# Kernel tuning notes

Measured on AMD Instinct MI355X. Metric: run time of the kernel, lower is better.

Reference implementation:

```python
import jax, jax.numpy as jnp
import numpy as np

B, P, TL = 2, 256, 1280          # batch, prefix len, text len
H, HEADS, HD = 1024, 16, 64      # hidden, heads, head_dim
NL, V = 2, 32000                 # layers, vocab


def layernorm(x, g, b, eps=1e-5):
    mu = jnp.mean(x, axis=-1, keepdims=True)
    var = jnp.mean((x - mu) ** 2, axis=-1, keepdims=True)
    return (x - mu) / jnp.sqrt(var + eps) * g + b


def setup_inputs() -> dict:
    key = jax.random.key(0)
    ks = jax.random.split(key, 12)
    s = 0.02
    return {
        "prefix_embeds": jax.random.normal(ks[0], (B, P, H), jnp.float32),
        "text_ids": jax.random.randint(ks[1], (B, TL), 0, V),
        "embed": jax.random.normal(ks[2], (V, H), jnp.float32) * s,
        "Wq": jax.random.normal(ks[3], (NL, H, H), jnp.float32) * s,
        "Wk": jax.random.normal(ks[4], (NL, H, H), jnp.float32) * s,
        "Wv": jax.random.normal(ks[5], (NL, H, H), jnp.float32) * s,
        "Wo": jax.random.normal(ks[6], (NL, H, H), jnp.float32) * s,
        "g1": jnp.ones((NL, H), jnp.float32),
        "b1": jnp.zeros((NL, H), jnp.float32),
        "g2": jnp.ones((NL, H), jnp.float32),
        "b2": jnp.zeros((NL, H), jnp.float32),
        "W1": jax.random.normal(ks[7], (NL, H, 4 * H), jnp.float32) * s,
        "bm1": jnp.zeros((NL, 4 * H), jnp.float32),
        "W2": jax.random.normal(ks[8], (NL, 4 * H, H), jnp.float32) * s,
        "bm2": jnp.zeros((NL, H), jnp.float32),
        "gf": jnp.ones((H,), jnp.float32),
        "bf": jnp.zeros((H,), jnp.float32),
        "Whead": jax.random.normal(ks[9], (H, V), jnp.float32) * s,
    }


def reference(prefix_embeds, text_ids, embed, Wq, Wk, Wv, Wo,
              g1, b1, g2, b2, W1, bm1, W2, bm2, gf, bf, Whead):
    x = jnp.concatenate([prefix_embeds, embed[text_ids]], axis=1)  # [B,T,H]
    T = x.shape[1]
    causal = jnp.tril(jnp.ones((T, T), dtype=bool))                # True = keep
    scale = 1.0 / jnp.sqrt(jnp.float32(HD))
    for l in range(NL):
        h = layernorm(x, g1[l], b1[l])
        q = (h @ Wq[l]).reshape(B, T, HEADS, HD).transpose(0, 2, 1, 3)
        k = (h @ Wk[l]).reshape(B, T, HEADS, HD).transpose(0, 2, 1, 3)
        v = (h @ Wv[l]).reshape(B, T, HEADS, HD).transpose(0, 2, 1, 3)
        scores = jnp.einsum('bhqd,bhkd->bhqk', q, k) * scale       # [B,h,T,T]
        scores = jnp.where(causal, scores, -jnp.inf)
        attn = jax.nn.softmax(scores, axis=-1)
        out = jnp.einsum('bhqk,bhkd->bhqd', attn, v)
        out = out.transpose(0, 2, 1, 3).reshape(B, T, H) @ Wo[l]
        x = x + out
        h2 = layernorm(x, g2[l], b2[l])
        x = x + jax.nn.silu(h2 @ W1[l] + bm1[l]) @ W2[l] + bm2[l]
    x = layernorm(x, gf, bf)
    return x @ Whead                                               # [B,T,V]
```

## Files before the change

kernel.cpp:

```cpp
#include <hip/hip_runtime.h>
#include <stdint.h>

#define B_ 2
#define P_ 256
#define TL_ 1280
#define T_ 1536
#define H_ 1024
#define HEADS_ 16
#define HD_ 64
#define NL_ 2
#define V_ 32000
#define F_ 4096
#define BT_ (B_ * T_)

typedef __attribute__((ext_vector_type(4))) float f32x4;
typedef __attribute__((ext_vector_type(8))) short short8;
typedef __attribute__((ext_vector_type(4))) short short4v;

typedef __attribute__((address_space(3))) uint32_t lds_u32_t;
typedef const __attribute__((address_space(1))) uint32_t glb_u32_t;

__device__ inline void gload_lds16(const void* g, void* l) {
    __builtin_amdgcn_global_load_lds((glb_u32_t*)g, (lds_u32_t*)l, 16, 0, 0);
}

__device__ inline short f2bf(float f) {
    union { float f; unsigned u; } v; v.f = f;
    unsigned r = v.u + 0x7FFF + ((v.u >> 16) & 1);
    return (short)(r >> 16);
}

#define BAR() asm volatile("s_barrier" ::: "memory")
#define WAIT_VM0() asm volatile("s_waitcnt vmcnt(0)" ::: "memory")
#define WAIT_VM4() asm volatile("s_waitcnt vmcnt(4)" ::: "memory")
#define WAIT_VM8() asm volatile("s_waitcnt vmcnt(8)" ::: "memory")
#define WAIT_VM32() asm volatile("s_waitcnt vmcnt(32)" ::: "memory")

__global__ __launch_bounds__(256) void k_cvt_all(
    const float* __restrict__ Wq, const float* __restrict__ Wk,
    const float* __restrict__ Wv, const float* __restrict__ Wo,
    const float* __restrict__ W1, const float* __restrict__ W2,
    const float* __restrict__ Wh,
    short* __restrict__ WqkvT, short* __restrict__ WoT,
    short* __restrict__ W1T, short* __restrict__ W2T, short* __restrict__ WhT) {
    int id = blockIdx.x;
    const float* src;
    short* dst;
    int K, N;
    float scale = 1.f;
    if (id < 6144) {
        int mat = id >> 10;
        int tile = id & 1023;
        int l = mat / 3, which = mat - l * 3;
        src = (which == 0 ? Wq : which == 1 ? Wk : Wv) + (size_t)l * H_ * H_;
        dst = WqkvT + (size_t)(l * 3 + which) * H_ * H_;
        K = H_; N = H_;
        if (which == 0) scale = 0.125f;
        id = tile;
    } else if (id < 8192) {
        int rel = id - 6144;
        int l = rel >> 10;
        src = Wo + (size_t)l * H_ * H_;
        dst = WoT + (size_t)l * H_ * H_;
        K = H_; N = H_;
        id = rel & 1023;
    } else if (id < 16384) {
        int rel = id - 8192;
        int l = rel >> 12;
        src = W1 + (size_t)l * H_ * F_;
        dst = W1T + (size_t)l * H_ * F_;
        K = H_; N = F_;
        id = rel & 4095;
    } else if (id < 24576) {
        int rel = id - 16384;
        int l = rel >> 12;
        src = W2 + (size_t)l * F_ * H_;
        dst = W2T + (size_t)l * F_ * H_;
        K = F_; N = H_;
        id = rel & 4095;
    } else {
        id -= 24576;
        src = Wh; dst = WhT;
        K = H_; N = V_;
    }
    int ntn = N >> 5;
    int nb = (id % ntn) * 32, kb = (id / ntn) * 32;

    __shared__ float ts[32][36];
    int tid = threadIdx.x;
    int r = tid >> 3, c4 = (tid & 7) * 4;
    f32x4 v = __builtin_nontemporal_load((const f32x4*)&src[(size_t)(kb + r) * N + nb + c4]);
    *(f32x4*)&ts[r][c4] = v;
    __syncthreads();
    int wn = tid >> 3, wk4 = (tid & 7) * 4;
    short o[4];
#pragma unroll
    for (int j = 0; j < 4; ++j) o[j] = f2bf(ts[wk4 + j][wn] * scale);
    *(short4v*)&dst[(size_t)(nb + wn) * K + kb + wk4] = *(short4v*)o;
}

__global__ __launch_bounds__(256) void k_embed_ln(const float* __restrict__ prefix,
                                                  const int* __restrict__ ids,
                                                  const float* __restrict__ emb,
                                                  const float* __restrict__ g,
                                                  const float* __restrict__ b,
                                                  float* __restrict__ x,
                                                  short* __restrict__ h) {
    int r = blockIdx.x;
    int bb = r / T_, t = r % T_;
    const float* src = (t < P_) ? (prefix + (size_t)(bb * P_ + t) * H_)
                                : (emb + (size_t)ids[bb * TL_ + (t - P_)] * H_);
    int tid = threadIdx.x;
    f32x4 v = *(const f32x4*)&src[tid * 4];
    *(f32x4*)&x[(size_t)r * H_ + tid * 4] = v;
    float s = v[0] + v[1] + v[2] + v[3];
    float sq = v[0] * v[0] + v[1] * v[1] + v[2] * v[2] + v[3] * v[3];
#pragma unroll
    for (int off = 32; off; off >>= 1) {
        s += __shfl_down(s, off, 64);
        sq += __shfl_down(sq, off, 64);
    }
    __shared__ float red[10];
    int wid = tid >> 6;
    if ((tid & 63) == 0) { red[wid] = s; red[4 + wid] = sq; }
    __syncthreads();
    if (tid == 0) {
        float S = red[0] + red[1] + red[2] + red[3];
        float SQ = red[4] + red[5] + red[6] + red[7];
        float mu = S * (1.0f / H_);
        float var = SQ * (1.0f / H_) - mu * mu;
        red[8] = mu;
        red[9] = rsqrtf(var + 1e-5f);
    }
    __syncthreads();
    float mu = red[8], rstd = red[9];
    short o[4];
#pragma unroll
    for (int j = 0; j < 4; ++j)
        o[j] = f2bf((v[j] - mu) * rstd * g[tid * 4 + j] + b[tid * 4 + j]);
    *(short4v*)&h[(size_t)r * H_ + tid * 4] = *(short4v*)o;
}

__global__ __launch_bounds__(256) void k_add_ln(float* __restrict__ x,
                                                const float* __restrict__ p,
                                                const float* __restrict__ g,
                                                const float* __restrict__ b,
                                                short* __restrict__ out) {
    int r = blockIdx.x;
    int tid = threadIdx.x;
    size_t base = (size_t)r * H_ + tid * 4;
    f32x4 v = *(f32x4*)&x[base];
#pragma unroll
    for (int sl = 0; sl < 4; ++sl) {
        f32x4 a = *(const f32x4*)&p[(size_t)sl * BT_ * H_ + base];
#pragma unroll
        for (int j = 0; j < 4; ++j) v[j] += a[j];
    }
    *(f32x4*)&x[base] = v;
    float s = v[0] + v[1] + v[2] + v[3];
    float sq = v[0] * v[0] + v[1] * v[1] + v[2] * v[2] + v[3] * v[3];
#pragma unroll
    for (int off = 32; off; off >>= 1) {
        s += __shfl_down(s, off, 64);
        sq += __shfl_down(sq, off, 64);
    }
    __shared__ float red[10];
    int wid = tid >> 6;
    if ((tid & 63) == 0) { red[wid] = s; red[4 + wid] = sq; }
    __syncthreads();
    if (tid == 0) {
        float S = red[0] + red[1] + red[2] + red[3];
        float SQ = red[4] + red[5] + red[6] + red[7];
        float mu = S * (1.0f / H_);
        float var = SQ * (1.0f / H_) - mu * mu;
        red[8] = mu;
        red[9] = rsqrtf(var + 1e-5f);
    }
    __syncthreads();
    float mu = red[8], rstd = red[9];
    short o[4];
#pragma unroll
    for (int j = 0; j < 4; ++j)
        o[j] = f2bf((v[j] - mu) * rstd * g[tid * 4 + j] + b[tid * 4 + j]);
    *(short4v*)&out[base] = *(short4v*)o;
}

template <int STORE, bool HAS_BIAS, bool SILU, int NSPLIT>
__global__ __launch_bounds__(256) void k_gemm(const short* __restrict__ A,
                                              const short* __restrict__ Bt,
                                              const float* __restrict__ bias,
                                              void* __restrict__ outp,
                                              void* __restrict__ outp2,
                                              void* __restrict__ outp3,
                                              int M, int N, int K, float alpha) {
    __shared__ short SH[32768];
    int tid = threadIdx.x;
    int lane = tid & 63, w = tid >> 6;
    int wr = w >> 1, wc = w & 1;
    int nwg = gridDim.x;
    int mblocks = M >> 7;
    int cpx = nwg >> 3;
    int logical = (blockIdx.x & 7) * cpx + (blockIdx.x >> 3);
    int ks = 0;
    if (NSPLIT > 1) {
        int per = mblocks * (N >> 7);
        ks = logical / per;
        logical -= ks * per;
    }
    int rp = logical % mblocks, cp = logical / mblocks;
    int mbase = rp * 128, nbase = cp * 128;
    int Kh = K / NSPLIT;
    int lr = lane & 15, hi = lane >> 4;
    int lg = hi * 4;

    f32x4 acc[4][4] = {};

    const short* Ab = A + (size_t)mbase * K + (size_t)ks * Kh;
    const short* Bb = Bt + (size_t)nbase * K + (size_t)ks * Kh;

    int koffb[2];
    koffb[0] = ((hi) ^ (lr & 7)) << 4;
    koffb[1] = ((4 + hi) ^ (lr & 7)) << 4;
    int arowb[4], browb[4];
#pragma unroll
    for (int m = 0; m < 4; ++m) arowb[m] = (wr * 64 + m * 16 + lr) * 128;
#pragma unroll
    for (int n = 0; n < 4; ++n) browb[n] = (wc * 64 + n * 16 + lr) * 128;

    auto stage = [&](int t, int buf) {
        short* la = SH + buf * 8192;
        short* lb = SH + 16384 + buf * 8192;
#pragma unroll
        for (int c = 0; c < 4; ++c) {
            int S = tid + 256 * c;
            int r = S >> 3, ch = S & 7;
            int gofs = t * 64 + ((ch ^ (r & 7)) << 3);
            gload_lds16(Ab + (size_t)r * K + gofs, la + S * 8);
            gload_lds16(Bb + (size_t)r * K + gofs, lb + S * 8);
        }
    };

    int NT = Kh >> 6;
    stage(0, 0);
    WAIT_VM0();
    BAR();

    for (int t = 0; t < NT; ++t) {
        if (t + 1 < NT) stage(t + 1, (t + 1) & 1);
        const char* a = (const char*)(SH + (t & 1) * 8192);
        const char* b = (const char*)(SH + 16384 + (t & 1) * 8192);
        short8 af[2][4], bfr[2][4];
#pragma unroll
        for (int kk = 0; kk < 2; ++kk) {
#pragma unroll
            for (int m = 0; m < 4; ++m) af[kk][m] = *(const short8*)(a + arowb[m] + koffb[kk]);
#pragma unroll
            for (int n = 0; n < 4; ++n) bfr[kk][n] = *(const short8*)(b + browb[n] + koffb[kk]);
        }
        __builtin_amdgcn_s_setprio(1);
#pragma unroll
        for (int kk = 0; kk < 2; ++kk)
#pragma unroll
            for (int m = 0; m < 4; ++m)
#pragma unroll
                for (int n = 0; n < 4; ++n)
                    acc[m][n] = __builtin_amdgcn_mfma_f32_16x16x32_bf16(af[kk][m], bfr[kk][n], acc[m][n], 0, 0, 0);
        __builtin_amdgcn_s_setprio(0);
        if (t + 1 < NT) {
            WAIT_VM0();
            BAR();
        }
    }

    if (STORE == 3 && nbase >= 2048) {
        BAR();
        short* Tt = SH;
#pragma unroll
        for (int ni = 0; ni < 4; ++ni) {
            int c2 = wc * 64 + ni * 16 + lr;
#pragma unroll
            for (int mi = 0; mi < 4; ++mi)
#pragma unroll
                for (int j = 0; j < 4; ++j)
                    Tt[c2 * 136 + wr * 64 + mi * 16 + lg + j] = f2bf(acc[mi][ni][j]);
        }
        BAR();
        int c2 = tid >> 1;
        int half = (tid & 1) * 64;
        int cc = (nbase + c2) & 1023;
        int head = cc >> 6, hd = cc & 63;
        int bb = mbase / T_;
        int t0 = mbase - bb * T_;
        short* dst = (short*)outp3 +
                     ((size_t)(bb * HEADS_ + head) * HD_ + hd) * T_ + t0 + half;
#pragma unroll
        for (int r8 = 0; r8 < 8; ++r8)
            *(short8*)&dst[r8 * 8] = *(short8*)&Tt[c2 * 136 + half + r8 * 8];
        return;
    }

#pragma unroll
    for (int ni = 0; ni < 4; ++ni) {
        int col = nbase + wc * 64 + ni * 16 + lr;
        float bv = (HAS_BIAS && ks == 0) ? bias[col] : 0.f;
#pragma unroll
        for (int mi = 0; mi < 4; ++mi) {
#pragma unroll
            for (int j = 0; j < 4; ++j) {
                int row = mbase + wr * 64 + mi * 16 + lg + j;
                float vv = acc[mi][ni][j] * alpha + bv;
                if (SILU) vv = vv / (1.f + __expf(-vv));
                if (STORE == 0) {
                    ((float*)outp)[(size_t)ks * M * N + (size_t)row * N + col] = vv;
                } else if (STORE == 1) {
                    ((short*)outp)[(size_t)row * N + col] = f2bf(vv);
                } else {
                    int seg = col >> 10;
                    int c = col & 1023;
                    if (seg == 0) {
                        ((short*)outp)[(size_t)row * H_ + c] = f2bf(vv);
                    } else {
                        ((short*)outp2)[(size_t)row * H_ + c] = f2bf(vv);
                    }
                }
            }
        }
    }
}

__global__ __launch_bounds__(512, 2) void k_gemm8(const short* __restrict__ A,
                                                  const short* __restrict__ Bt,
                                                  float* __restrict__ C,
                                                  int M, int N, int K) {
    __shared__ short As[2 * 256 * 64];
    __shared__ short Bs[2 * 256 * 64];
    int tid = threadIdx.x;
    int lane = tid & 63, w = tid >> 6;
    int wr = w >> 2, wc = w & 3;
    int lr = lane & 15, hi = lane >> 4;

    int mtiles = M >> 8;
    int total = mtiles * (N >> 8);
    int g = ((blockIdx.x & 7) << 5) + (blockIdx.x >> 3);
    int qq = total >> 8, rr = total & 255;
    int start = g * qq + (g < rr ? g : rr);
    int cnt = qq + (g < rr ? 1 : 0);

    int r0 = tid >> 3;
    int gcol = ((tid & 7) ^ (r0 & 7)) * 8;
    int koff0 = (hi * 16) ^ ((lr & 7) << 4);
    int koff1 = (64 + hi * 16) ^ ((lr & 7) << 4);
    int arow[8], brow[4];
#pragma unroll
    for (int m = 0; m < 8; ++m) arow[m] = (wr * 128 + m * 16 + lr) * 128;
#pragma unroll
    for (int n = 0; n < 4; ++n) brow[n] = (wc * 64 + n * 16 + lr) * 128;

    f32x4 acc[8][4];
    short8 aF[4][2], bF[4][2];
    const char* Ac = (const char*)As;
    const char* Bc = (const char*)Bs;

    auto stage = [&](const short* Gb, char* Lb, int tau, int hf) {
        const short* g0 = Gb + (size_t)(hf * 128 + r0) * K + tau * 64 + gcol;
        char* l = Lb + (tau & 1) * 32768 + hf * 16384;
        gload_lds16(g0, l + tid * 16);
        gload_lds16(g0 + (size_t)64 * K, l + (tid + 512) * 16);
    };
    auto prolog = [&](const short* Ab, const short* Bb) {
        stage(Ab, (char*)As, 0, 0); stage(Ab, (char*)As, 0, 1);
        stage(Bb, (char*)Bs, 0, 0); stage(Bb, (char*)Bs, 0, 1);
        stage(Ab, (char*)As, 1, 0); stage(Ab, (char*)As, 1, 1);
        stage(Bb, (char*)Bs, 1, 0); stage(Bb, (char*)Bs, 1, 1);
    };
    auto lda4 = [&](const char* base, int roff) {
#pragma unroll
        for (int m = 0; m < 4; ++m) {
            aF[m][0] = *(const short8*)(base + arow[roff + m] + koff0);
            aF[m][1] = *(const short8*)(base + arow[roff + m] + koff1);
        }
    };
    auto ldb2 = [&](const char* base, int noff) {
#pragma unroll
        for (int n = 0; n < 2; ++n) {
            bF[noff + n][0] = *(const short8*)(base + brow[noff + n] + koff0);
            bF[noff + n][1] = *(const short8*)(base + brow[noff + n] + koff1);
        }
    };

#define MFMA_QUAD(MOFF, NOFF)                                                          \
    __builtin_amdgcn_s_setprio(1);                                                     \
    _Pragma("unroll") for (int m = 0; m < 4; ++m) {                                    \
        _Pragma("unroll") for (int n = 0; n < 2; ++n) {                                \
            acc[MOFF + m][NOFF + n] = __builtin_amdgcn_mfma_f32_16x16x32_bf16(         \
                aF[m][0], bF[NOFF + n][0], acc[MOFF + m][NOFF + n], 0, 0, 0);          \
            acc[MOFF + m][NOFF + n] = __builtin_amdgcn_mfma_f32_16x16x32_bf16(         \
                aF[m][1], bF[NOFF + n][1], acc[MOFF + m][NOFF + n], 0, 0, 0);          \
        }                                                                              \
    }                                                                                  \
    __builtin_amdgcn_s_setprio(0);

    int NK = K >> 6;
    int niters = NK >> 1;

    for (int i = 0; i < cnt; ++i) {
        int t0 = start + i;
        int rp = t0 % mtiles, cp = t0 / mtiles;
        const short* Ab = A + (size_t)rp * 256 * K;
        const short* Bb = Bt + (size_t)cp * 256 * K;
        f32x4 zz = {0.f, 0.f, 0.f, 0.f};
#pragma unroll
        for (int m = 0; m < 8; ++m)
#pragma unroll
            for (int n = 0; n < 4; ++n) acc[m][n] = zz;

        if (i == 0) {
            prolog(Ab, Bb);
            WAIT_VM0();
            BAR();
        }

        for (int it = 0; it < niters; ++it) {
            bool st = it < niters - 1;
            int u2 = 2 * it + 2, v2 = 2 * it + 3;
            const char* a0 = Ac;            const char* b0 = Bc;
            const char* a1 = Ac + 32768;    const char* b1 = Bc + 32768;

            lda4(a0, 0); ldb2(b0, 0);
            BAR();
            MFMA_QUAD(0, 0);
            BAR();
            ldb2(b0, 2);
            BAR();
            MFMA_QUAD(0, 2);
            BAR();
            lda4(a0, 4);
            if (st) stage(Bb, (char*)Bs, u2, 0);
            BAR();
            MFMA_QUAD(4, 0);
            BAR();
            if (st) stage(Bb, (char*)Bs, u2, 1);
            BAR();
            MFMA_QUAD(4, 2);
            if (st) { WAIT_VM4(); } else { WAIT_VM0(); }
            BAR();

            lda4(a1, 0); ldb2(b1, 0);
            if (st) stage(Ab, (char*)As, u2, 0);
            BAR();
            MFMA_QUAD(0, 0);
            BAR();
            ldb2(b1, 2);
            if (st) stage(Ab, (char*)As, u2, 1);
            BAR();
            MFMA_QUAD(0, 2);
            BAR();
            lda4(a1, 4);
            if (st) stage(Bb, (char*)Bs, v2, 0);
            BAR();
            MFMA_QUAD(4, 0);
            BAR();
            if (st) { stage(Bb, (char*)Bs, v2, 1); stage(Ab, (char*)As, v2, 0); stage(Ab, (char*)As, v2, 1); }
            BAR();
            MFMA_QUAD(4, 2);
            if (st) { WAIT_VM8(); } else { WAIT_VM0(); }
            BAR();
        }

        bool more = (i + 1 < cnt);
        if (more) {
            int t1 = t0 + 1;
            int rp1 = t1 % mtiles, cp1 = t1 / mtiles;
            prolog(A + (size_t)rp1 * 256 * K, Bt + (size_t)cp1 * 256 * K);
        }
        int crow = rp * 256 + wr * 128 + hi * 4;
        int ccol = cp * 256 + wc * 64 + lr;
#pragma unroll
        for (int m = 0; m < 8; ++m)
#pragma unroll
            for (int n = 0; n < 4; ++n) {
#pragma unroll
                for (int j = 0; j < 4; ++j)
                    C[(size_t)(crow + m * 16 + j) * N + ccol + n * 16] = acc[m][n][j];
            }
        if (more) {
            WAIT_VM32();
            BAR();
        }
    }
#undef MFMA_QUAD
}

__global__ __launch_bounds__(256) void k_attn(const short* __restrict__ q,
                                              const short* __restrict__ k,
                                              const short* __restrict__ vT,
                                              short* __restrict__ out) {
    int qt = blockIdx.x, head = blockIdx.y, b = blockIdx.z;
    int qbase = qt * 64;
    __shared__ short Qs[64][72];
    __shared__ short Ps[4][16][72];
    int tid = threadIdx.x, lane = tid & 63, w = tid >> 6;
    int lr = lane & 15, lg4 = (lane >> 4) * 4, lk8 = (lane >> 4) * 8;

#pragma unroll
    for (int c = 0; c < 2; ++c) {
        int chunk = tid + 256 * c;
        int row = chunk >> 3, h8 = (chunk & 7) * 8;
        *(short8*)&Qs[row][h8] =
            *(const short8*)&q[(size_t)(b * T_ + qbase + row) * H_ + head * HD_ + h8];
    }
    __syncthreads();

    short8 qf[2];
    qf[0] = *(short8*)&Qs[w * 16 + lr][lk8];
    qf[1] = *(short8*)&Qs[w * 16 + lr][32 + lk8];

    f32x4 o[4] = {};
    float lsum[4] = {0.f, 0.f, 0.f, 0.f};

    for (int kt = 0; kt <= qt; ++kt) {
        int kb = kt * 64;
        f32x4 s[4] = {};
#pragma unroll
        for (int ks = 0; ks < 2; ++ks) {
#pragma unroll
            for (int f = 0; f < 4; ++f) {
                short8 kf = *(const short8*)&k[(size_t)(b * T_ + kb + f * 16 + lr) * H_ +
                                               head * HD_ + ks * 32 + lk8];
                s[f] = __builtin_amdgcn_mfma_f32_16x16x32_bf16(qf[ks], kf, s[f], 0, 0, 0);
            }
        }
        if (kt == qt) {
#pragma unroll
            for (int f = 0; f < 4; ++f) {
                int key = kb + f * 16 + lr;
#pragma unroll
                for (int j = 0; j < 4; ++j) {
                    int qrow = qbase + w * 16 + lg4 + j;
                    if (key > qrow) s[f][j] = -1e30f;
                }
            }
        }
#pragma unroll
        for (int j = 0; j < 4; ++j) {
            float rs = 0.f;
#pragma unroll
            for (int f = 0; f < 4; ++f) {
                float p = __expf(fminf(s[f][j], 60.f));
                s[f][j] = p;
                rs += p;
            }
#pragma unroll
            for (int off = 1; off < 16; off <<= 1) rs += __shfl_xor(rs, off, 64);
            lsum[j] += rs;
#pragma unroll
            for (int f = 0; f < 4; ++f) Ps[w][lg4 + j][f * 16 + lr] = f2bf(s[f][j]);
        }
#pragma unroll
        for (int ks2 = 0; ks2 < 2; ++ks2) {
            short8 pf = *(short8*)&Ps[w][lr][ks2 * 32 + lk8];
            __builtin_amdgcn_s_setprio(1);
#pragma unroll
            for (int f = 0; f < 4; ++f) {
                short8 vf = *(const short8*)&vT[((size_t)(b * HEADS_ + head) * HD_ + f * 16 + lr) * T_ +
                                                kb + ks2 * 32 + lk8];
                o[f] = __builtin_amdgcn_mfma_f32_16x16x32_bf16(pf, vf, o[f], 0, 0, 0);
            }
            __builtin_amdgcn_s_setprio(0);
        }
    }
#pragma unroll
    for (int f = 0; f < 4; ++f)
#pragma unroll
        for (int j = 0; j < 4; ++j) {
            float val = o[f][j] / lsum[j];
            out[(size_t)(b * T_ + qbase + w * 16 + lg4 + j) * H_ + head * HD_ + f * 16 + lr] =
                f2bf(val);
        }
}

extern "C" void kernel_launch(void* const* d_in, const int* in_sizes, int n_in,
                              void* d_out, int out_size, void* d_ws, size_t ws_size,
                              hipStream_t stream) {
    const float* prefix = (const float*)d_in[0];
    const int* ids = (const int*)d_in[1];
    const float* emb = (const float*)d_in[2];
    const float* Wq = (const float*)d_in[3];
    const float* Wk = (const float*)d_in[4];
    const float* Wv = (const float*)d_in[5];
    const float* Wo = (const float*)d_in[6];
    const float* g1 = (const float*)d_in[7];
    const float* b1 = (const float*)d_in[8];
    const float* g2 = (const float*)d_in[9];
    const float* b2 = (const float*)d_in[10];
    const float* W1 = (const float*)d_in[11];
    const float* bm1 = (const float*)d_in[12];
    const float* W2 = (const float*)d_in[13];
    const float* bm2 = (const float*)d_in[14];
    const float* gf = (const float*)d_in[15];
    const float* bf = (const float*)d_in[16];
    const float* Whead = (const float*)d_in[17];
    float* out = (float*)d_out;

    char* wsp = (char*)d_ws;
    float* x = (float*)wsp;   wsp += (size_t)BT_ * H_ * 4;
    float* p = (float*)wsp;   wsp += (size_t)4 * BT_ * H_ * 4;
    short* h = (short*)wsp;   wsp += (size_t)BT_ * H_ * 2;
    short* qb = (short*)wsp;  wsp += (size_t)BT_ * H_ * 2;
    short* kb = (short*)wsp;  wsp += (size_t)BT_ * H_ * 2;
    short* vT = (short*)wsp;  wsp += (size_t)BT_ * H_ * 2;
    short* ao = (short*)wsp;  wsp += (size_t)BT_ * H_ * 2;
    short* mid = (short*)wsp; wsp += (size_t)BT_ * F_ * 2;
    short* WqkvT = (short*)wsp; wsp += (size_t)NL_ * 3 * H_ * H_ * 2;
    short* WoT = (short*)wsp;   wsp += (size_t)NL_ * H_ * H_ * 2;
    short* W1T = (short*)wsp;   wsp += (size_t)NL_ * H_ * F_ * 2;
    short* W2T = (short*)wsp;   wsp += (size_t)NL_ * F_ * H_ * 2;
    short* WhT = (short*)wsp;   wsp += (size_t)H_ * V_ * 2;

    dim3 blk(256);
    k_cvt_all<<<dim3(56576), blk, 0, stream>>>(Wq, Wk, Wv, Wo, W1, W2, Whead,
                                               WqkvT, WoT, W1T, W2T, WhT);
    k_embed_ln<<<BT_, blk, 0, stream>>>(prefix, ids, emb, g1, b1, x, h);
    for (int l = 0; l < NL_; ++l) {
        size_t o1 = (size_t)l * H_ * H_;
        size_t oq = (size_t)l * 3 * H_ * H_;
        size_t o2 = (size_t)l * H_ * F_;
        k_gemm<3, false, false, 1><<<dim3(576), blk, 0, stream>>>(
            h, WqkvT + oq, nullptr, qb, kb, vT, BT_, 3 * H_, H_, 1.f);
        k_attn<<<dim3(T_ / 64, HEADS_, B_), blk, 0, stream>>>(qb, kb, vT, ao);
        k_gemm<0, false, false, 4><<<dim3(768), blk, 0, stream>>>(
            ao, WoT + o1, nullptr, p, nullptr, nullptr, BT_, H_, H_, 1.f);
        k_add_ln<<<BT_, blk, 0, stream>>>(x, p, g2 + l * H_, b2 + l * H_, h);
        k_gemm<1, true, true, 1><<<dim3(768), blk, 0, stream>>>(
            h, W1T + o2, bm1 + (size_t)l * F_, mid, nullptr, nullptr, BT_, F_, H_, 1.f);
        k_gemm<0, true, false, 4><<<dim3(768), blk, 0, stream>>>(
            mid, W2T + o2, bm2 + (size_t)l * H_, p, nullptr, nullptr, BT_, H_, F_, 1.f);
        const float* gn = (l + 1 < NL_) ? g1 + (l + 1) * H_ : gf;
        const float* bn = (l + 1 < NL_) ? b1 + (l + 1) * H_ : bf;
        k_add_ln<<<BT_, blk, 0, stream>>>(x, p, gn, bn, h);
    }
    k_gemm8<<<dim3(256), dim3(512), 0, stream>>>(h, WhT, out, BT_, V_, H_);
}
```

Before: 828.2 us.

## Replace head GEMM with 128x256-tile kernel and defer attention row-sum reduction

Adds a new LM-head GEMM kernel that uses 128x256 tiles with K-step 32, double-buffered LDS staging via global_load_lds, and 4 blocks per CU. It is launched over 3000 tiles instead of the persistent 256-block 256x256 kernel, aiming for better occupancy and load balance on the large output. Separately, the attention kernel now accumulates per-lane partial row sums and does the cross-lane shuffle reduction once after the key loop instead of every iteration. The smaller tiles reduce operand reuse per block, and the grid size hardcodes the tile count for M=3072, N=32000.

```diff
diff --git a/kernel.cpp b/kernel.cpp
--- a/kernel.cpp
+++ b/kernel.cpp
@@ -328,6 +328,84 @@
     }
 }
 
+__global__ __launch_bounds__(512, 4) void k_gemmh(const short* __restrict__ A,
+                                                  const short* __restrict__ Bt,
+                                                  float* __restrict__ C,
+                                                  int M, int N, int K) {
+    __shared__ short As[2][128 * 32];
+    __shared__ short Bs[2][256 * 32];
+    int tid = threadIdx.x;
+    int lane = tid & 63, w = tid >> 6;
+    int wr = w >> 2, wc = w & 3;
+    int lr = lane & 15, hi = lane >> 4;
+
+    int mtiles = M >> 7;
+    int logical = (blockIdx.x & 7) * (gridDim.x >> 3) + (blockIdx.x >> 3);
+    int rp = logical % mtiles, cp = logical / mtiles;
+    const short* Ab = A + (size_t)rp * 128 * K;
+    const short* Bb = Bt + (size_t)cp * 256 * K;
+
+    int koff = ((hi ^ (lr & 3)) << 4);
+    int arow[4], brow[4];
+#pragma unroll
+    for (int m = 0; m < 4; ++m) arow[m] = (wr * 64 + m * 16 + lr) * 64;
+#pragma unroll
+    for (int n = 0; n < 4; ++n) brow[n] = (wc * 64 + n * 16 + lr) * 64;
+
+    f32x4 acc[4][4] = {};
+
+    int rA = tid >> 2, cA = tid & 3;
+    int gA = ((cA ^ (rA & 3)) << 3);
+
+    auto stage = [&](int t, int buf) {
+        gload_lds16(Ab + (size_t)rA * K + t * 32 + gA, (char*)&As[buf][0] + tid * 16);
+#pragma unroll
+        for (int c = 0; c < 2; ++c) {
+            int S = tid + 512 * c;
+            int rB = S >> 2, cB = S & 3;
+            int gB = t * 32 + ((cB ^ (rB & 3)) << 3);
+            gload_lds16(Bb + (size_t)rB * K + gB, (char*)&Bs[buf][0] + S * 16);
+        }
+    };
+
+    int NT = K >> 5;
+    stage(0, 0);
+    WAIT_VM0();
+    BAR();
+
+    for (int t = 0; t < NT; ++t) {
+        if (t + 1 < NT) stage(t + 1, (t + 1) & 1);
+        const char* a = (const char*)&As[t & 1][0];
+        const char* b = (const char*)&Bs[t & 1][0];
+        short8 af[4], bfr[4];
+#pragma unroll
+        for (int m = 0; m < 4; ++m) af[m] = *(const short8*)(a + arow[m] + koff);
+#pragma unroll
+        for (int n = 0; n < 4; ++n) bfr[n] = *(const short8*)(b + brow[n] + koff);
+        __builtin_amdgcn_s_setprio(1);
+#pragma unroll
+        for (int m = 0; m < 4; ++m)
+#pragma unroll
+            for (int n = 0; n < 4; ++n)
+                acc[m][n] = __builtin_amdgcn_mfma_f32_16x16x32_bf16(af[m], bfr[n], acc[m][n], 0, 0, 0);
+        __builtin_amdgcn_s_setprio(0);
+        if (t + 1 < NT) {
+            WAIT_VM0();
+            BAR();
+        }
+    }
+
+    int crow = rp * 128 + wr * 64 + hi * 4;
+    int ccol = cp * 256 + wc * 64 + lr;
+#pragma unroll
+    for (int m = 0; m < 4; ++m)
+#pragma unroll
+        for (int n = 0; n < 4; ++n)
+#pragma unroll
+            for (int j = 0; j < 4; ++j)
+                C[(size_t)(crow + m * 16 + j) * N + ccol + n * 16] = acc[m][n][j];
+}
+
 __global__ __launch_bounds__(512, 2) void k_gemm8(const short* __restrict__ A,
                                                   const short* __restrict__ Bt,
                                                   float* __restrict__ C,
@@ -543,16 +621,12 @@
         }
 #pragma unroll
         for (int j = 0; j < 4; ++j) {
-            float rs = 0.f;
 #pragma unroll
             for (int f = 0; f < 4; ++f) {
                 float p = __expf(fminf(s[f][j], 60.f));
                 s[f][j] = p;
-                rs += p;
+                lsum[j] += p;
             }
-#pragma unroll
-            for (int off = 1; off < 16; off <<= 1) rs += __shfl_xor(rs, off, 64);
-            lsum[j] += rs;
 #pragma unroll
             for (int f = 0; f < 4; ++f) Ps[w][lg4 + j][f * 16 + lr] = f2bf(s[f][j]);
         }
@@ -568,6 +642,11 @@
             }
             __builtin_amdgcn_s_setprio(0);
         }
+    }
+#pragma unroll
+    for (int j = 0; j < 4; ++j) {
+#pragma unroll
+        for (int off = 1; off < 16; off <<= 1) lsum[j] += __shfl_xor(lsum[j], off, 64);
     }
 #pragma unroll
     for (int f = 0; f < 4; ++f)
@@ -639,5 +718,5 @@
         const float* bn = (l + 1 < NL_) ? b1 + (l + 1) * H_ : bf;
         k_add_ln<<<BT_, blk, 0, stream>>>(x, p, gn, bn, h);
     }
-    k_gemm8<<<dim3(256), dim3(512), 0, stream>>>(h, WhT, out, BT_, V_, H_);
-}
+    k_gemmh<<<dim3(3000), dim3(512), 0, stream>>>(h, WhT, out, BT_, V_, H_);
+}
```

Result: slower. 876.0 us (+5.8%).
